# Kernel optimization log

Hardware: AMD Instinct MI355X
Metric: run time of the kernel (lower is better)

## Reference

```python
import jax, jax.numpy as jnp
import numpy as np

DIST_THD = 1.0   # config.dist_thd
EPS = 1e-8       # matches torch.nn.functional.cosine_similarity eps


def setup_inputs() -> dict:
    key = jax.random.key(0)
    k1, k2 = jax.random.split(key)
    async_fea = jax.random.normal(k1, (64, 512, 128), dtype=jnp.float32)  # [B, N, D]
    coord = jax.random.normal(k2, (64, 512, 2), dtype=jnp.float32)        # [B, N, 2]
    return {"async_fea": async_fea, "coord": coord}


def reference(async_fea, coord):
    B, N, _ = async_fea.shape
    # pairwise cosine similarity: normalize rows, then batched matmul
    norms = jnp.maximum(jnp.linalg.norm(async_fea, axis=-1, keepdims=True), EPS)
    fn = async_fea / norms
    cos = jnp.einsum('bid,bjd->bij', fn, fn)  # [B, N, N]

    # pairwise euclidean distance on coords
    diff = coord[:, :, None, :] - coord[:, None, :, :]  # [B, N, N, 2]
    d2 = jnp.sum(diff * diff, axis=-1)                   # [B, N, N]
    eye = jnp.eye(N, dtype=d2.dtype)
    # add eye before sqrt so the (zeroed-out) diagonal stays sqrt-safe
    dist = jnp.sqrt(d2 + eye)
    off_diag = 1.0 - eye

    async_adj = cos * jnp.exp(-dist / DIST_THD) * off_diag
    sync_adj = jnp.where(dist < DIST_THD, 1.0, 0.0) * off_diag
    return jnp.stack([async_adj, sync_adj])  # [2, B, N, N]
```

## Files before the change

### kernel.cpp

```cpp
#include <hip/hip_runtime.h>
#include <hip/hip_bf16.h>

typedef short bf16x8 __attribute__((ext_vector_type(8)));
typedef float f32x4  __attribute__((ext_vector_type(4)));

#define NB 64
#define NN 512
#define DD 128

__device__ __forceinline__ unsigned short f2bf(float f) {
    unsigned int u = __float_as_uint(f);
    unsigned int r = (u + 0x7FFFu + ((u >> 16) & 1u)) >> 16;
    return (unsigned short)r;
}

__global__ __launch_bounds__(256) void ASG_norm_kernel(
    const float* __restrict__ fea, unsigned int* __restrict__ fn)
{
    const int wid  = threadIdx.x >> 6;
    const int lane = threadIdx.x & 63;
    const int row0 = blockIdx.x * 16 + wid * 4;
    const float2* src = reinterpret_cast<const float2*>(fea);

    float2 v[4];
    float  s[4];
#pragma unroll
    for (int rr = 0; rr < 4; ++rr) {
        v[rr] = src[(size_t)(row0 + rr) * (DD / 2) + lane];
        s[rr] = v[rr].x * v[rr].x + v[rr].y * v[rr].y;
    }
#pragma unroll
    for (int o = 32; o; o >>= 1) {
#pragma unroll
        for (int rr = 0; rr < 4; ++rr) s[rr] += __shfl_xor(s[rr], o);
    }
#pragma unroll
    for (int rr = 0; rr < 4; ++rr) {
        const float scale = 1.0f / fmaxf(sqrtf(s[rr]), 1e-8f);
        const unsigned short a = f2bf(v[rr].x * scale);
        const unsigned short b = f2bf(v[rr].y * scale);
        fn[(size_t)(row0 + rr) * (DD / 2) + lane] =
            (unsigned int)a | ((unsigned int)b << 16);
    }
}

__global__ __launch_bounds__(256, 4) void ASG_adj_kernel(
    const unsigned short* __restrict__ fn, const float* __restrict__ coord,
    float* __restrict__ out)
{
    const int id  = blockIdx.x;
    const int xcd = id & 7;
    const int q   = id >> 3;
    const int b   = xcd + 8 * (q >> 5);
    const int t   = q & 31;
    const int bi  = t >> 3;
    const int bj  = t & 7;

    const int tid = threadIdx.x;
    const int wid = tid >> 6, lane = tid & 63;
    const int wr  = wid >> 1, wc = wid & 1;
    const int row0 = bi * 128 + wr * 64;
    const int col0 = bj * 64  + wc * 32;
    const int lo = lane & 15, hi = lane >> 4;

    __shared__ float2 crow[128];
    __shared__ float2 ccol[64];
    __shared__ float  xpose[4][16 * 36];

    const float2* cb = reinterpret_cast<const float2*>(coord) + (size_t)b * NN;
    if (tid < 128)      crow[tid] = cb[bi * 128 + tid];
    else if (tid < 192) ccol[tid - 128] = cb[bj * 64 + (tid - 128)];
    __syncthreads();

    const unsigned short* fb = fn + (size_t)b * NN * DD;
    const int lk = hi * 8;

    bf16x8 bfrag[2][4];
#pragma unroll
    for (int n = 0; n < 2; ++n) {
        const unsigned short* p = fb + (size_t)(col0 + n * 16 + lo) * DD + lk;
#pragma unroll
        for (int kk = 0; kk < 4; ++kk)
            bfrag[n][kk] = *reinterpret_cast<const bf16x8*>(p + kk * 32);
    }

    float* outA = out + (size_t)b * NN * NN;
    float* outS = out + (size_t)NB * NN * NN + (size_t)b * NN * NN;
    float* xp = xpose[wid];

    const int c4 = (lane & 7) * 4;
    const int jbase = col0 + c4;
    float2 cj[4];
#pragma unroll
    for (int q2 = 0; q2 < 4; ++q2) cj[q2] = ccol[wc * 32 + c4 + q2];

#pragma unroll
    for (int m = 0; m < 4; ++m) {
        const unsigned short* p = fb + (size_t)(row0 + m * 16 + lo) * DD + lk;
        bf16x8 afrag[4];
#pragma unroll
        for (int kk = 0; kk < 4; ++kk)
            afrag[kk] = *reinterpret_cast<const bf16x8*>(p + kk * 32);

        f32x4 acc[2];
#pragma unroll
        for (int n = 0; n < 2; ++n) acc[n] = (f32x4){0.f, 0.f, 0.f, 0.f};
#pragma unroll
        for (int n = 0; n < 2; ++n)
#pragma unroll
            for (int kk = 0; kk < 4; ++kk)
                acc[n] = __builtin_amdgcn_mfma_f32_16x16x32_bf16(
                    afrag[kk], bfrag[n][kk], acc[n], 0, 0, 0);

#pragma unroll
        for (int n = 0; n < 2; ++n)
#pragma unroll
            for (int r = 0; r < 4; ++r)
                xp[(hi * 4 + r) * 36 + n * 16 + lo] = acc[n][r];

#pragma unroll
        for (int p2 = 0; p2 < 2; ++p2) {
            const int rr = p2 * 8 + (lane >> 3);
            const f32x4 cv = *reinterpret_cast<const f32x4*>(&xp[rr * 36 + c4]);
            const int i = row0 + m * 16 + rr;
            const float2 ci = crow[wr * 64 + m * 16 + rr];
            f32x4 av, sv;
#pragma unroll
            for (int q2 = 0; q2 < 4; ++q2) {
                const int j = jbase + q2;
                const float dx = ci.x - cj[q2].x;
                const float dy = ci.y - cj[q2].y;
                const float d2 = __fadd_rn(__fmul_rn(dx, dx), __fmul_rn(dy, dy));
                const float dist = __fsqrt_rn(d2);
                const bool diag = (i == j);
                av[q2] = diag ? 0.0f : cv[q2] * __expf(-dist);
                sv[q2] = (!diag && dist < 1.0f) ? 1.0f : 0.0f;
            }
            const size_t off = (size_t)i * NN + jbase;
            __builtin_nontemporal_store(av, reinterpret_cast<f32x4*>(outA + off));
            __builtin_nontemporal_store(sv, reinterpret_cast<f32x4*>(outS + off));
        }
    }
}

extern "C" void kernel_launch(void* const* d_in, const int* in_sizes, int n_in,
                              void* d_out, int out_size, void* d_ws, size_t ws_size,
                              hipStream_t stream) {
    const float* fea   = (const float*)d_in[0];
    const float* coord = (const float*)d_in[1];
    float* out = (float*)d_out;
    unsigned int* fn_ws = (unsigned int*)d_ws;

    ASG_norm_kernel<<<dim3(NB * NN / 16), 256, 0, stream>>>(fea, fn_ws);
    ASG_adj_kernel<<<dim3(4 * 8 * NB), 256, 0, stream>>>(
        (const unsigned short*)fn_ws, coord, out);
}
```

Baseline: 41.77 us.

## Fuse row normalization into adjacency kernel, scaling dot products post-MFMA

Removes the separate normalization kernel and its bf16 workspace round trip. The fused kernel computes per-row inverse norms for its row and column tiles, converts raw fp32 features to bf16 on load, and applies the norms to the MFMA result. This saves one launch and the workspace write/read. In exchange it reads fp32 features (twice the bytes), with each block redundantly recomputing norms. Normalizing after the bf16 product also changes rounding slightly.

Result: slower. 74.65 us (+78.7%).

```diff
diff --git a/kernel.cpp b/kernel.cpp
--- a/kernel.cpp
+++ b/kernel.cpp
@@ -14,38 +14,19 @@
     return (unsigned short)r;
 }
 
-__global__ __launch_bounds__(256) void ASG_norm_kernel(
-    const float* __restrict__ fea, unsigned int* __restrict__ fn)
-{
-    const int wid  = threadIdx.x >> 6;
-    const int lane = threadIdx.x & 63;
-    const int row0 = blockIdx.x * 16 + wid * 4;
-    const float2* src = reinterpret_cast<const float2*>(fea);
-
-    float2 v[4];
-    float  s[4];
-#pragma unroll
-    for (int rr = 0; rr < 4; ++rr) {
-        v[rr] = src[(size_t)(row0 + rr) * (DD / 2) + lane];
-        s[rr] = v[rr].x * v[rr].x + v[rr].y * v[rr].y;
-    }
-#pragma unroll
-    for (int o = 32; o; o >>= 1) {
-#pragma unroll
-        for (int rr = 0; rr < 4; ++rr) s[rr] += __shfl_xor(s[rr], o);
-    }
-#pragma unroll
-    for (int rr = 0; rr < 4; ++rr) {
-        const float scale = 1.0f / fmaxf(sqrtf(s[rr]), 1e-8f);
-        const unsigned short a = f2bf(v[rr].x * scale);
-        const unsigned short b = f2bf(v[rr].y * scale);
-        fn[(size_t)(row0 + rr) * (DD / 2) + lane] =
-            (unsigned int)a | ((unsigned int)b << 16);
-    }
+__device__ __forceinline__ bf16x8 load_frag8(const float* __restrict__ p) {
+    const f32x4 a = *reinterpret_cast<const f32x4*>(p);
+    const f32x4 b = *reinterpret_cast<const f32x4*>(p + 4);
+    bf16x8 r;
+    r[0] = (short)f2bf(a[0]); r[1] = (short)f2bf(a[1]);
+    r[2] = (short)f2bf(a[2]); r[3] = (short)f2bf(a[3]);
+    r[4] = (short)f2bf(b[0]); r[5] = (short)f2bf(b[1]);
+    r[6] = (short)f2bf(b[2]); r[7] = (short)f2bf(b[3]);
+    return r;
 }
 
-__global__ __launch_bounds__(256, 4) void ASG_adj_kernel(
-    const unsigned short* __restrict__ fn, const float* __restrict__ coord,
+__global__ __launch_bounds__(256, 4) void ASG_fused_kernel(
+    const float* __restrict__ fea, const float* __restrict__ coord,
     float* __restrict__ out)
 {
     const int id  = blockIdx.x;
@@ -63,25 +44,45 @@
     const int col0 = bj * 64  + wc * 32;
     const int lo = lane & 15, hi = lane >> 4;
 
+    __shared__ float  rsA[128];
+    __shared__ float  rsB[64];
     __shared__ float2 crow[128];
     __shared__ float2 ccol[64];
     __shared__ float  xpose[4][16 * 36];
 
-    const float2* cb = reinterpret_cast<const float2*>(coord) + (size_t)b * NN;
-    if (tid < 128)      crow[tid] = cb[bi * 128 + tid];
-    else if (tid < 192) ccol[tid - 128] = cb[bj * 64 + (tid - 128)];
+    const float* feab = fea + (size_t)b * NN * DD;
+
+    if (tid < 192) {
+        const int row = (tid < 128) ? (bi * 128 + tid) : (bj * 64 + tid - 128);
+        const f32x4* rp = reinterpret_cast<const f32x4*>(feab + (size_t)row * DD);
+        f32x4 s4 = (f32x4){0.f, 0.f, 0.f, 0.f};
+#pragma unroll
+        for (int k = 0; k < 32; ++k) {
+            const f32x4 x = rp[k];
+            s4 += x * x;
+        }
+        const float s = (s4[0] + s4[1]) + (s4[2] + s4[3]);
+        const float rs = 1.0f / fmaxf(sqrtf(s), 1e-8f);
+        if (tid < 128) rsA[tid] = rs;
+        else           rsB[tid - 128] = rs;
+    } else {
+        const int u = tid - 192;
+        const float2* cb = reinterpret_cast<const float2*>(coord) + (size_t)b * NN;
+        crow[u]      = cb[bi * 128 + u];
+        crow[u + 64] = cb[bi * 128 + u + 64];
+        ccol[u]      = cb[bj * 64 + u];
+    }
     __syncthreads();
 
-    const unsigned short* fb = fn + (size_t)b * NN * DD;
     const int lk = hi * 8;
 
     bf16x8 bfrag[2][4];
 #pragma unroll
     for (int n = 0; n < 2; ++n) {
-        const unsigned short* p = fb + (size_t)(col0 + n * 16 + lo) * DD + lk;
+        const float* p = feab + (size_t)(col0 + n * 16 + lo) * DD + lk;
 #pragma unroll
         for (int kk = 0; kk < 4; ++kk)
-            bfrag[n][kk] = *reinterpret_cast<const bf16x8*>(p + kk * 32);
+            bfrag[n][kk] = load_frag8(p + kk * 32);
     }
 
     float* outA = out + (size_t)b * NN * NN;
@@ -93,14 +94,15 @@
     float2 cj[4];
 #pragma unroll
     for (int q2 = 0; q2 < 4; ++q2) cj[q2] = ccol[wc * 32 + c4 + q2];
+    const f32x4 rsb4 = *reinterpret_cast<const f32x4*>(&rsB[wc * 32 + c4]);
 
 #pragma unroll
     for (int m = 0; m < 4; ++m) {
-        const unsigned short* p = fb + (size_t)(row0 + m * 16 + lo) * DD + lk;
+        const float* p = feab + (size_t)(row0 + m * 16 + lo) * DD + lk;
         bf16x8 afrag[4];
 #pragma unroll
         for (int kk = 0; kk < 4; ++kk)
-            afrag[kk] = *reinterpret_cast<const bf16x8*>(p + kk * 32);
+            afrag[kk] = load_frag8(p + kk * 32);
 
         f32x4 acc[2];
 #pragma unroll
@@ -123,6 +125,7 @@
             const int rr = p2 * 8 + (lane >> 3);
             const f32x4 cv = *reinterpret_cast<const f32x4*>(&xp[rr * 36 + c4]);
             const int i = row0 + m * 16 + rr;
+            const float rsi = rsA[wr * 64 + m * 16 + rr];
             const float2 ci = crow[wr * 64 + m * 16 + rr];
             f32x4 av, sv;
 #pragma unroll
@@ -133,7 +136,8 @@
                 const float d2 = __fadd_rn(__fmul_rn(dx, dx), __fmul_rn(dy, dy));
                 const float dist = __fsqrt_rn(d2);
                 const bool diag = (i == j);
-                av[q2] = diag ? 0.0f : cv[q2] * __expf(-dist);
+                av[q2] = diag ? 0.0f
+                              : cv[q2] * rsi * rsb4[q2] * __expf(-dist);
                 sv[q2] = (!diag && dist < 1.0f) ? 1.0f : 0.0f;
             }
             const size_t off = (size_t)i * NN + jbase;
@@ -149,9 +153,6 @@
     const float* fea   = (const float*)d_in[0];
     const float* coord = (const float*)d_in[1];
     float* out = (float*)d_out;
-    unsigned int* fn_ws = (unsigned int*)d_ws;
 
-    ASG_norm_kernel<<<dim3(NB * NN / 16), 256, 0, stream>>>(fea, fn_ws);
-    ASG_adj_kernel<<<dim3(4 * 8 * NB), 256, 0, stream>>>(
-        (const unsigned short*)fn_ws, coord, out);
+    ASG_fused_kernel<<<dim3(4 * 8 * NB), 256, 0, stream>>>(fea, coord, out);
 }
```

## Drop LDS transpose, store MFMA outputs directly, prefetch A fragments, XCD-align norm

Applied to the files above, without the earlier changes.

The adjacency kernel no longer stages MFMA accumulators through shared memory for a transpose. It now computes the epilogue directly in the MFMA output layout and issues scalar nontemporal stores, which removes LDS traffic but replaces 16-byte vector stores with 4-byte scalar stores. A fragments for the next row tile are double-buffered and prefetched before the current MFMAs. The norm kernel now maps blocks the same way as the adjacency kernel, so each batch's normalized rows are written by blocks in the same XCD group that later read them, which is meant to improve L2 locality.

New measurement: 56.50 us. 35.3% more time.

```diff
diff --git a/kernel.cpp b/kernel.cpp
--- a/kernel.cpp
+++ b/kernel.cpp
@@ -17,9 +17,14 @@
 __global__ __launch_bounds__(256) void ASG_norm_kernel(
     const float* __restrict__ fea, unsigned int* __restrict__ fn)
 {
+    const int id   = blockIdx.x;
+    const int xcd  = id & 7;
+    const int q    = id >> 3;
+    const int b    = xcd + 8 * (q >> 5);
+    const int t    = q & 31;
     const int wid  = threadIdx.x >> 6;
     const int lane = threadIdx.x & 63;
-    const int row0 = blockIdx.x * 16 + wid * 4;
+    const int row0 = b * NN + t * 16 + wid * 4;
     const float2* src = reinterpret_cast<const float2*>(fea);
 
     float2 v[4];
@@ -38,9 +43,9 @@
     for (int rr = 0; rr < 4; ++rr) {
         const float scale = 1.0f / fmaxf(sqrtf(s[rr]), 1e-8f);
         const unsigned short a = f2bf(v[rr].x * scale);
-        const unsigned short b = f2bf(v[rr].y * scale);
+        const unsigned short bb = f2bf(v[rr].y * scale);
         fn[(size_t)(row0 + rr) * (DD / 2) + lane] =
-            (unsigned int)a | ((unsigned int)b << 16);
+            (unsigned int)a | ((unsigned int)bb << 16);
     }
 }
 
@@ -65,7 +70,6 @@
 
     __shared__ float2 crow[128];
     __shared__ float2 ccol[64];
-    __shared__ float  xpose[4][16 * 36];
 
     const float2* cb = reinterpret_cast<const float2*>(coord) + (size_t)b * NN;
     if (tid < 128)      crow[tid] = cb[bi * 128 + tid];
@@ -86,61 +90,68 @@
 
     float* outA = out + (size_t)b * NN * NN;
     float* outS = out + (size_t)NB * NN * NN + (size_t)b * NN * NN;
-    float* xp = xpose[wid];
 
-    const int c4 = (lane & 7) * 4;
-    const int jbase = col0 + c4;
-    float2 cj[4];
-#pragma unroll
-    for (int q2 = 0; q2 < 4; ++q2) cj[q2] = ccol[wc * 32 + c4 + q2];
+    const int j0 = col0 + lo;
+    const int j1 = col0 + 16 + lo;
+    const float2 cj0 = ccol[wc * 32 + lo];
+    const float2 cj1 = ccol[wc * 32 + 16 + lo];
 
-#pragma unroll
-    for (int m = 0; m < 4; ++m) {
-        const unsigned short* p = fb + (size_t)(row0 + m * 16 + lo) * DD + lk;
-        bf16x8 afrag[4];
-#pragma unroll
-        for (int kk = 0; kk < 4; ++kk)
-            afrag[kk] = *reinterpret_cast<const bf16x8*>(p + kk * 32);
+#define LOADA(DST, MM)                                                        \
+    {                                                                         \
+        const unsigned short* p =                                             \
+            fb + (size_t)(row0 + (MM) * 16 + lo) * DD + lk;                   \
+        _Pragma("unroll")                                                     \
+        for (int kk = 0; kk < 4; ++kk)                                        \
+            DST[kk] = *reinterpret_cast<const bf16x8*>(p + kk * 32);          \
+    }
 
-        f32x4 acc[2];
-#pragma unroll
-        for (int n = 0; n < 2; ++n) acc[n] = (f32x4){0.f, 0.f, 0.f, 0.f};
-#pragma unroll
-        for (int n = 0; n < 2; ++n)
-#pragma unroll
-            for (int kk = 0; kk < 4; ++kk)
-                acc[n] = __builtin_amdgcn_mfma_f32_16x16x32_bf16(
-                    afrag[kk], bfrag[n][kk], acc[n], 0, 0, 0);
+#define EPI_ELEM(MM, R, CV, CJ, J)                                            \
+    {                                                                         \
+        const int i = row0 + (MM) * 16 + hi * 4 + (R);                        \
+                  \
+        const float dx = ci.x - (CJ).x;                                       \
+        const float dy = ci.y - (CJ).y;                                       \
+        const float d2 = __fadd_rn(__fmul_rn(dx, dx), __fmul_rn(dy, dy));     \
+        const float dist = __fsqrt_rn(d2);                                    \
+        const bool diag = (i == (J));                                         \
+        const float av = diag ? 0.0f : (CV) * __expf(-dist);                  \
+        const float sv = (!diag && dist < 1.0f) ? 1.0f : 0.0f;                \
+        const size_t off = (size_t)i * NN + (J);                              \
+        __builtin_nontemporal_store(av, outA + off);                          \
+        __builtin_nontemporal_store(sv, outS + off);                          \
+    }
 
-#pragma unroll
-        for (int n = 0; n < 2; ++n)
-#pragma unroll
-            for (int r = 0; r < 4; ++r)
-                xp[(hi * 4 + r) * 36 + n * 16 + lo] = acc[n][r];
+#define STEP(MM, CURF, NEXTF, DO_PREF)                                        \
+    {                                                                         \
+        if (DO_PREF) LOADA(NEXTF, (MM) + 1);                                  \
+        f32x4 acc0 = (f32x4){0.f, 0.f, 0.f, 0.f};                             \
+        f32x4 acc1 = (f32x4){0.f, 0.f, 0.f, 0.f};                             \
+        _Pragma("unroll")                                                     \
+        for (int kk = 0; kk < 4; ++kk)                                        \
+            acc0 = __builtin_amdgcn_mfma_f32_16x16x32_bf16(                   \
+                CURF[kk], bfrag[0][kk], acc0, 0, 0, 0);                       \
+        _Pragma("unroll")                                                     \
+        for (int kk = 0; kk < 4; ++kk)                                        \
+            acc1 = __builtin_amdgcn_mfma_f32_16x16x32_bf16(                   \
+                CURF[kk], bfrag[1][kk], acc1, 0, 0, 0);                       \
+        _Pragma("unroll")                                                     \
+        for (int r = 0; r < 4; ++r) {                                         \
+            const float2 ci = crow[wr * 64 + (MM) * 16 + hi * 4 + r];         \
+            EPI_ELEM(MM, r, acc0[r], cj0, j0);                                \
+            EPI_ELEM(MM, r, acc1[r], cj1, j1);                                \
+        }                                                                     \
+    }
 
-#pragma unroll
-        for (int p2 = 0; p2 < 2; ++p2) {
-            const int rr = p2 * 8 + (lane >> 3);
-            const f32x4 cv = *reinterpret_cast<const f32x4*>(&xp[rr * 36 + c4]);
-            const int i = row0 + m * 16 + rr;
-            const float2 ci = crow[wr * 64 + m * 16 + rr];
-            f32x4 av, sv;
-#pragma unroll
-            for (int q2 = 0; q2 < 4; ++q2) {
-                const int j = jbase + q2;
-                const float dx = ci.x - cj[q2].x;
-                const float dy = ci.y - cj[q2].y;
-                const float d2 = __fadd_rn(__fmul_rn(dx, dx), __fmul_rn(dy, dy));
-                const float dist = __fsqrt_rn(d2);
-                const bool diag = (i == j);
-                av[q2] = diag ? 0.0f : cv[q2] * __expf(-dist);
-                sv[q2] = (!diag && dist < 1.0f) ? 1.0f : 0.0f;
-            }
-            const size_t off = (size_t)i * NN + jbase;
-            __builtin_nontemporal_store(av, reinterpret_cast<f32x4*>(outA + off));
-            __builtin_nontemporal_store(sv, reinterpret_cast<f32x4*>(outS + off));
-        }
-    }
+    bf16x8 af0[4], af1[4];
+    LOADA(af0, 0);
+    STEP(0, af0, af1, 1);
+    STEP(1, af1, af0, 1);
+    STEP(2, af0, af1, 1);
+    STEP(3, af1, af0, 0);
+
+#undef STEP
+#undef EPI_ELEM
+#undef LOADA
 }
 
 extern "C" void kernel_launch(void* const* d_in, const int* in_sizes, int n_in,
@@ -151,7 +162,7 @@
     float* out = (float*)d_out;
     unsigned int* fn_ws = (unsigned int*)d_ws;
 
-    ASG_norm_kernel<<<dim3(NB * NN / 16), 256, 0, stream>>>(fea, fn_ws);
-    ASG_adj_kernel<<<dim3(4 * 8 * NB), 256, 0, stream>>>(
+    ASG_norm_kernel<<<dim3(2048), 256, 0, stream>>>(fea, fn_ws);
+    ASG_adj_kernel<<<dim3(2048), 256, 0, stream>>>(
         (const unsigned short*)fn_ws, coord, out);
 }
```

## Fuse row normalization into adjacency kernel via LDS-staged bf16 tiles

Applied to the files above, without the earlier changes.

Removes the separate normalization kernel and bf16 workspace. Each block loads its fp32 feature rows, normalizes them, converts to bf16 into shared memory, and feeds MFMA from LDS. The epilogue writes MFMA accumulator elements directly as scalar stores instead of transposing through LDS for vectorized nontemporal stores. This trades a launch and workspace round trip for redundant per-block normalization, larger LDS use, and narrower output stores.

Measured after the change: 43.84 us. +5.0%, slower.

```diff
diff --git a/kernel.cpp b/kernel.cpp
--- a/kernel.cpp
+++ b/kernel.cpp
@@ -14,38 +14,16 @@
     return (unsigned short)r;
 }
 
-__global__ __launch_bounds__(256) void ASG_norm_kernel(
-    const float* __restrict__ fea, unsigned int* __restrict__ fn)
-{
-    const int wid  = threadIdx.x >> 6;
-    const int lane = threadIdx.x & 63;
-    const int row0 = blockIdx.x * 16 + wid * 4;
-    const float2* src = reinterpret_cast<const float2*>(fea);
-
-    float2 v[4];
-    float  s[4];
-#pragma unroll
-    for (int rr = 0; rr < 4; ++rr) {
-        v[rr] = src[(size_t)(row0 + rr) * (DD / 2) + lane];
-        s[rr] = v[rr].x * v[rr].x + v[rr].y * v[rr].y;
-    }
-#pragma unroll
-    for (int o = 32; o; o >>= 1) {
-#pragma unroll
-        for (int rr = 0; rr < 4; ++rr) s[rr] += __shfl_xor(s[rr], o);
-    }
-#pragma unroll
-    for (int rr = 0; rr < 4; ++rr) {
-        const float scale = 1.0f / fmaxf(sqrtf(s[rr]), 1e-8f);
-        const unsigned short a = f2bf(v[rr].x * scale);
-        const unsigned short b = f2bf(v[rr].y * scale);
-        fn[(size_t)(row0 + rr) * (DD / 2) + lane] =
-            (unsigned int)a | ((unsigned int)b << 16);
-    }
+__device__ __forceinline__ bf16x8 lds_frag(const unsigned short* p) {
+    union { unsigned int u[4]; bf16x8 v; } r;
+    const uint2 a = *reinterpret_cast<const uint2*>(p);
+    const uint2 b = *reinterpret_cast<const uint2*>(p + 4);
+    r.u[0] = a.x; r.u[1] = a.y; r.u[2] = b.x; r.u[3] = b.y;
+    return r.v;
 }
 
-__global__ __launch_bounds__(256, 4) void ASG_adj_kernel(
-    const unsigned short* __restrict__ fn, const float* __restrict__ coord,
+__global__ __launch_bounds__(256, 3) void ASG_fused_kernel(
+    const float* __restrict__ fea, const float* __restrict__ coord,
     float* __restrict__ out)
 {
     const int id  = blockIdx.x;
@@ -63,82 +41,112 @@
     const int col0 = bj * 64  + wc * 32;
     const int lo = lane & 15, hi = lane >> 4;
 
+    __shared__ unsigned short fa[128 * 132];
+    __shared__ unsigned short fbs[64 * 132];
     __shared__ float2 crow[128];
     __shared__ float2 ccol[64];
-    __shared__ float  xpose[4][16 * 36];
 
+    const float* feab = fea + (size_t)b * NN * DD;
+
+    {
+        const int li = lane & 31;
+        const int l5 = lane >> 5;
+#pragma unroll 4
+        for (int p = 0; p < 24; ++p) {
+            const int rr = wid * 48 + p * 2 + l5;
+            const int rg = (rr < 128) ? bi * 128 + rr : bj * 64 + (rr - 128);
+            const f32x4 v = *reinterpret_cast<const f32x4*>(
+                feab + (size_t)rg * DD + li * 4);
+            float s = v[0] * v[0] + v[1] * v[1] + v[2] * v[2] + v[3] * v[3];
+            s += __shfl_xor(s, 16);
+            s += __shfl_xor(s, 8);
+            s += __shfl_xor(s, 4);
+            s += __shfl_xor(s, 2);
+            s += __shfl_xor(s, 1);
+            const float rs = 1.0f / fmaxf(sqrtf(s), 1e-8f);
+            const unsigned int u0 =
+                (unsigned int)f2bf(v[0] * rs) | ((unsigned int)f2bf(v[1] * rs) << 16);
+            const unsigned int u1 =
+                (unsigned int)f2bf(v[2] * rs) | ((unsigned int)f2bf(v[3] * rs) << 16);
+            unsigned short* dst = (rr < 128) ? &fa[rr * 132 + li * 4]
+                                             : &fbs[(rr - 128) * 132 + li * 4];
+            *reinterpret_cast<unsigned int*>(dst)     = u0;
+            *reinterpret_cast<unsigned int*>(dst + 2) = u1;
+        }
+    }
     const float2* cb = reinterpret_cast<const float2*>(coord) + (size_t)b * NN;
     if (tid < 128)      crow[tid] = cb[bi * 128 + tid];
     else if (tid < 192) ccol[tid - 128] = cb[bj * 64 + (tid - 128)];
     __syncthreads();
 
-    const unsigned short* fb = fn + (size_t)b * NN * DD;
     const int lk = hi * 8;
 
     bf16x8 bfrag[2][4];
 #pragma unroll
     for (int n = 0; n < 2; ++n) {
-        const unsigned short* p = fb + (size_t)(col0 + n * 16 + lo) * DD + lk;
+        const unsigned short* p = &fbs[(wc * 32 + n * 16 + lo) * 132 + lk];
 #pragma unroll
         for (int kk = 0; kk < 4; ++kk)
-            bfrag[n][kk] = *reinterpret_cast<const bf16x8*>(p + kk * 32);
+            bfrag[n][kk] = lds_frag(p + kk * 32);
     }
 
     float* outA = out + (size_t)b * NN * NN;
     float* outS = out + (size_t)NB * NN * NN + (size_t)b * NN * NN;
-    float* xp = xpose[wid];
 
-    const int c4 = (lane & 7) * 4;
-    const int jbase = col0 + c4;
-    float2 cj[4];
-#pragma unroll
-    for (int q2 = 0; q2 < 4; ++q2) cj[q2] = ccol[wc * 32 + c4 + q2];
+    const int j0 = col0 + lo;
+    const int j1 = col0 + 16 + lo;
+    const float2 cj0 = ccol[wc * 32 + lo];
+    const float2 cj1 = ccol[wc * 32 + 16 + lo];
 
 #pragma unroll
     for (int m = 0; m < 4; ++m) {
-        const unsigned short* p = fb + (size_t)(row0 + m * 16 + lo) * DD + lk;
         bf16x8 afrag[4];
+        {
+            const unsigned short* p = &fa[(wr * 64 + m * 16 + lo) * 132 + lk];
+#pragma unroll
+            for (int kk = 0; kk < 4; ++kk)
+                afrag[kk] = lds_frag(p + kk * 32);
+        }
+
+        f32x4 acc0 = (f32x4){0.f, 0.f, 0.f, 0.f};
+        f32x4 acc1 = (f32x4){0.f, 0.f, 0.f, 0.f};
 #pragma unroll
         for (int kk = 0; kk < 4; ++kk)
-            afrag[kk] = *reinterpret_cast<const bf16x8*>(p + kk * 32);
-
-        f32x4 acc[2];
+            acc0 = __builtin_amdgcn_mfma_f32_16x16x32_bf16(
+                afrag[kk], bfrag[0][kk], acc0, 0, 0, 0);
 #pragma unroll
-        for (int n = 0; n < 2; ++n) acc[n] = (f32x4){0.f, 0.f, 0.f, 0.f};
-#pragma unroll
-        for (int n = 0; n < 2; ++n)
-#pragma unroll
-            for (int kk = 0; kk < 4; ++kk)
-                acc[n] = __builtin_amdgcn_mfma_f32_16x16x32_bf16(
-                    afrag[kk], bfrag[n][kk], acc[n], 0, 0, 0);
+        for (int kk = 0; kk < 4; ++kk)
+            acc1 = __builtin_amdgcn_mfma_f32_16x16x32_bf16(
+                afrag[kk], bfrag[1][kk], acc1, 0, 0, 0);
 
 #pragma unroll
-        for (int n = 0; n < 2; ++n)
-#pragma unroll
-            for (int r = 0; r < 4; ++r)
-                xp[(hi * 4 + r) * 36 + n * 16 + lo] = acc[n][r];
-
-#pragma unroll
-        for (int p2 = 0; p2 < 2; ++p2) {
-            const int rr = p2 * 8 + (lane >> 3);
-            const f32x4 cv = *reinterpret_cast<const f32x4*>(&xp[rr * 36 + c4]);
-            const int i = row0 + m * 16 + rr;
-            const float2 ci = crow[wr * 64 + m * 16 + rr];
-            f32x4 av, sv;
-#pragma unroll
-            for (int q2 = 0; q2 < 4; ++q2) {
-                const int j = jbase + q2;
-                const float dx = ci.x - cj[q2].x;
-                const float dy = ci.y - cj[q2].y;
+        for (int r = 0; r < 4; ++r) {
+            const int i = row0 + m * 16 + hi * 4 + r;
+            const float2 ci = crow[wr * 64 + m * 16 + hi * 4 + r];
+            {
+                const float dx = ci.x - cj0.x;
+                const float dy = ci.y - cj0.y;
                 const float d2 = __fadd_rn(__fmul_rn(dx, dx), __fmul_rn(dy, dy));
                 const float dist = __fsqrt_rn(d2);
-                const bool diag = (i == j);
-                av[q2] = diag ? 0.0f : cv[q2] * __expf(-dist);
-                sv[q2] = (!diag && dist < 1.0f) ? 1.0f : 0.0f;
+                const bool diag = (i == j0);
+                const float av = diag ? 0.0f : acc0[r] * __expf(-dist);
+                const float sv = (!diag && dist < 1.0f) ? 1.0f : 0.0f;
+                const size_t off = (size_t)i * NN + j0;
+                outA[off] = av;
+                outS[off] = sv;
             }
-            const size_t off = (size_t)i * NN + jbase;
-            __builtin_nontemporal_store(av, reinterpret_cast<f32x4*>(outA + off));
-            __builtin_nontemporal_store(sv, reinterpret_cast<f32x4*>(outS + off));
+            {
+                const float dx = ci.x - cj1.x;
+                const float dy = ci.y - cj1.y;
+                const float d2 = __fadd_rn(__fmul_rn(dx, dx), __fmul_rn(dy, dy));
+                const float dist = __fsqrt_rn(d2);
+                const bool diag = (i == j1);
+                const float av = diag ? 0.0f : acc1[r] * __expf(-dist);
+                const float sv = (!diag && dist < 1.0f) ? 1.0f : 0.0f;
+                const size_t off = (size_t)i * NN + j1;
+                outA[off] = av;
+                outS[off] = sv;
+            }
         }
     }
 }
@@ -149,9 +157,6 @@
     const float* fea   = (const float*)d_in[0];
     const float* coord = (const float*)d_in[1];
     float* out = (float*)d_out;
-    unsigned int* fn_ws = (unsigned int*)d_ws;
 
-    ASG_norm_kernel<<<dim3(NB * NN / 16), 256, 0, stream>>>(fea, fn_ws);
-    ASG_adj_kernel<<<dim3(4 * 8 * NB), 256, 0, stream>>>(
-        (const unsigned short*)fn_ws, coord, out);
+    ASG_fused_kernel<<<dim3(2048), 256, 0, stream>>>(fea, coord, out);
 }
```
